# Kernel optimization log

Hardware: AMD Instinct MI355X
Metric: run time of the kernel (lower is better)

## Reference

```python
import jax, jax.numpy as jnp
import numpy as np


def _cdist(x, y):
    # Euclidean (p=2) pairwise distances, matching torch.cdist.
    # x: [B, N, D], y: [B, M, D] -> [B, N, M]
    xx = jnp.sum(x * x, axis=-1)                      # [B, N]
    yy = jnp.sum(y * y, axis=-1)                      # [B, M]
    zz = jnp.einsum('bnd,bmd->bnm', x, y)             # [B, N, M]
    d2 = xx[:, :, None] + yy[:, None, :] - 2.0 * zz
    return jnp.sqrt(jnp.maximum(d2, 0.0))


def setup_inputs() -> dict:
    key = jax.random.key(0)
    k1, k2 = jax.random.split(key)
    gts = jax.random.normal(k1, (4, 8192, 3), dtype=jnp.float32)
    preds = jax.random.normal(k2, (4, 8192, 3), dtype=jnp.float32)
    return {"gts": gts, "preds": preds}


def reference(gts, preds):
    P = _cdist(gts, preds)                 # [B, N, M]
    loss_1 = jnp.sum(jnp.min(P, axis=1), axis=1)  # min over gts points, sum over preds
    loss_2 = jnp.sum(jnp.min(P, axis=2), axis=1)  # min over preds points, sum over gts
    return loss_1 + loss_2                 # [B]
```

## Files before the change

kernel.cpp:

```cpp
#include <hip/hip_runtime.h>
#include <math.h>

#define BB 4
#define NPTS 8192
#define THREADS 256
#define NQ_TOTAL (2 * BB * NPTS)
#define SLICES 4
#define RPS (NPTS / SLICES)
#define QPW 32
#define QPB_MIN (4 * QPW)
#define QGROUPS (NPTS / QPB_MIN)
#define NBLK_MIN (SLICES * 2 * BB * QGROUPS)

typedef __attribute__((ext_vector_type(8)))  short bf16x8;
typedef __attribute__((ext_vector_type(16))) float f32x16;


__device__ __forceinline__ unsigned short f2bf(float f) {
    unsigned u = __float_as_uint(f);
    u += 0x7FFF + ((u >> 16) & 1);
    return (unsigned short)(u >> 16);
}
__device__ __forceinline__ float bf2f(unsigned short h) {
    return __uint_as_float(((unsigned)h) << 16);
}

__global__ __launch_bounds__(THREADS) void pack_kernel(
    const float* __restrict__ gts, const float* __restrict__ preds,
    uint4* __restrict__ refpack, uint4* __restrict__ qpack,
    float* __restrict__ out) {
    int idx = blockIdx.x * THREADS + threadIdx.x;
    if (idx < BB) out[idx] = 0.0f;
    if (idx >= NQ_TOTAL) return;
    int set  = idx / (BB * NPTS);
    int pidx = idx - set * (BB * NPTS);
    const float* src = set ? preds : gts;
    unsigned short hx = f2bf(src[pidx * 3 + 0]);
    unsigned short hy = f2bf(src[pidx * 3 + 1]);
    unsigned short hz = f2bf(src[pidx * 3 + 2]);
    float fx = bf2f(hx), fy = bf2f(hy), fz = bf2f(hz);
    float rr = fmaf(fx, fx, fmaf(fy, fy, fz * fz));
    unsigned short hrr = f2bf(rr);
    unsigned short hlo = f2bf(rr - bf2f(hrr));
    const unsigned short ONE = 0x3F80;

    uint4 rv;
    rv.x = (unsigned)hx  | ((unsigned)hy  << 16);
    rv.y = (unsigned)hz  | ((unsigned)hrr << 16);
    rv.z = (unsigned)hlo | ((unsigned)ONE << 16);
    rv.w = (unsigned)ONE;
    refpack[idx] = rv;

    unsigned short nx = f2bf(-2.0f * fx);
    unsigned short ny = f2bf(-2.0f * fy);
    unsigned short nz = f2bf(-2.0f * fz);
    uint4 qv;
    qv.x = (unsigned)nx  | ((unsigned)ny  << 16);
    qv.y = (unsigned)nz  | ((unsigned)ONE << 16);
    qv.z = (unsigned)ONE | ((unsigned)hrr << 16);
    qv.w = (unsigned)hlo;
    qpack[idx] = qv;
}

__global__ __launch_bounds__(THREADS) void min_kernel(
    const uint4* __restrict__ refpack, const uint4* __restrict__ qpack,
    float* __restrict__ minpart) {
    __shared__ uint4 sref[RPS];

    int tid   = threadIdx.x;
    int blk   = blockIdx.x;
    int slice = blk >> 9;
    int rem   = blk & 511;
    int dir   = rem >> 8;
    int b     = (rem >> 6) & 3;
    int qg    = rem & 63;
    int qset  = dir ^ 1;
    int rset  = dir;

    const uint4* rgl = refpack + (size_t)(rset * BB + b) * NPTS
                     + (size_t)slice * RPS;
    #pragma unroll
    for (int i = 0; i < RPS / THREADS; ++i)
        sref[i * THREADS + tid] = rgl[i * THREADS + tid];
    __syncthreads();

    int wid  = tid >> 6;
    int lane = tid & 63;
    int l31  = lane & 31;
    int half = lane >> 5;

    size_t qoff = (size_t)(qset * BB + b) * NPTS + (size_t)qg * QPB_MIN
                + (size_t)wid * QPW;
    bf16x8 bq = {0, 0, 0, 0, 0, 0, 0, 0};
    if (lane < 32) bq = ((const bf16x8*)qpack)[qoff + l31];

    f32x16 zeroc;
    #pragma unroll
    for (int r = 0; r < 16; ++r) zeroc[r] = 0.0f;

    float macc0 = 3.0e38f, macc1 = 3.0e38f;

    const bf16x8* sp = (const bf16x8*)sref;
    #pragma unroll 4
    for (int t = 0; t < RPS / 64; ++t) {
        bf16x8 a0 = sp[t * 64 + l31];
        bf16x8 a1 = sp[t * 64 + 32 + l31];
        f32x16 d0 = __builtin_amdgcn_mfma_f32_32x32x16_bf16(a0, bq, zeroc, 0, 0, 0);
        f32x16 d1 = __builtin_amdgcn_mfma_f32_32x32x16_bf16(a1, bq, zeroc, 0, 0, 0);
        #pragma unroll
        for (int r = 0; r < 16; r += 2) {
            macc0 = fminf(fminf(d0[r], d0[r + 1]), macc0);
            macc1 = fminf(fminf(d1[r], d1[r + 1]), macc1);
        }
    }

    float macc = fminf(macc0, macc1);
    macc = fminf(macc, __shfl_xor(macc, 32, 64));

    float* mp = minpart + (size_t)slice * NQ_TOTAL
              + (size_t)(dir * BB + b) * NPTS + (size_t)qg * QPB_MIN
              + (size_t)wid * QPW;
    if (lane < 32) mp[l31] = macc;
}

__global__ __launch_bounds__(THREADS) void merge_kernel(
    const float* __restrict__ minpart, float* __restrict__ out) {
    int q = blockIdx.x * THREADS + threadIdx.x;
    float m = minpart[q];
    #pragma unroll
    for (int s = 1; s < SLICES; ++s)
        m = fminf(m, minpart[(size_t)s * NQ_TOTAL + q]);
    float d = sqrtf(fmaxf(m, 0.0f));
    int b = (q >> 13) & 3;

    float sum = d;
    #pragma unroll
    for (int off = 32; off > 0; off >>= 1)
        sum += __shfl_down(sum, off, 64);

    __shared__ float wsum[THREADS / 64];
    int lane = threadIdx.x & 63;
    int wid  = threadIdx.x >> 6;
    if (lane == 0) wsum[wid] = sum;
    __syncthreads();
    if (threadIdx.x == 0)
        atomicAdd(out + b, wsum[0] + wsum[1] + wsum[2] + wsum[3]);
}

extern "C" void kernel_launch(void* const* d_in, const int* in_sizes, int n_in,
                              void* d_out, int out_size, void* d_ws, size_t ws_size,
                              hipStream_t stream) {
    const float* gts   = (const float*)d_in[0];
    const float* preds = (const float*)d_in[1];
    float* out = (float*)d_out;

    char* ws = (char*)d_ws;
    uint4* refpack = (uint4*)ws;
    uint4* qpack   = (uint4*)(ws + (size_t)NQ_TOTAL * 16);
    float* minpart = (float*)(ws + (size_t)NQ_TOTAL * 32);

    pack_kernel<<<NQ_TOTAL / THREADS, THREADS, 0, stream>>>(
        gts, preds, refpack, qpack, out);

    min_kernel<<<NBLK_MIN, THREADS, 0, stream>>>(refpack, qpack, minpart);

    merge_kernel<<<NQ_TOTAL / THREADS, THREADS, 0, stream>>>(minpart, out);
}
```

Baseline: 83.48 us.

## Process 64 queries per wave to reuse each LDS reference load across two MFMAs

Each wave now handles two 32-query B-fragments, so every pair of reference A-fragments read from LDS feeds four MFMAs instead of two. This halves the number of blocks and the total LDS traffic and staging of reference slices per query. In exchange it raises accumulator register pressure (four 16-wide results in flight), lowers the unroll to 2, and halves the grid, which may reduce occupancy and latency hiding.

```diff
diff --git a/kernel.cpp b/kernel.cpp
--- a/kernel.cpp
+++ b/kernel.cpp
@@ -7,7 +7,7 @@
 #define NQ_TOTAL (2 * BB * NPTS)
 #define SLICES 4
 #define RPS (NPTS / SLICES)
-#define QPW 32
+#define QPW 64
 #define QPB_MIN (4 * QPW)
 #define QGROUPS (NPTS / QPB_MIN)
 #define NBLK_MIN (SLICES * 2 * BB * QGROUPS)
@@ -69,11 +69,11 @@
 
     int tid   = threadIdx.x;
     int blk   = blockIdx.x;
-    int slice = blk >> 9;
-    int rem   = blk & 511;
-    int dir   = rem >> 8;
-    int b     = (rem >> 6) & 3;
-    int qg    = rem & 63;
+    int slice = blk >> 8;
+    int rem   = blk & 255;
+    int dir   = rem >> 7;
+    int b     = (rem >> 5) & 3;
+    int qg    = rem & 31;
     int qset  = dir ^ 1;
     int rset  = dir;
 
@@ -87,40 +87,52 @@
     int wid  = tid >> 6;
     int lane = tid & 63;
     int l31  = lane & 31;
-    int half = lane >> 5;
 
     size_t qoff = (size_t)(qset * BB + b) * NPTS + (size_t)qg * QPB_MIN
                 + (size_t)wid * QPW;
-    bf16x8 bq = {0, 0, 0, 0, 0, 0, 0, 0};
-    if (lane < 32) bq = ((const bf16x8*)qpack)[qoff + l31];
+    bf16x8 bq0 = {0, 0, 0, 0, 0, 0, 0, 0};
+    bf16x8 bq1 = {0, 0, 0, 0, 0, 0, 0, 0};
+    if (lane < 32) {
+        bq0 = ((const bf16x8*)qpack)[qoff + l31];
+        bq1 = ((const bf16x8*)qpack)[qoff + 32 + l31];
+    }
 
     f32x16 zeroc;
     #pragma unroll
     for (int r = 0; r < 16; ++r) zeroc[r] = 0.0f;
 
-    float macc0 = 3.0e38f, macc1 = 3.0e38f;
+    float m00 = 3.0e38f, m01 = 3.0e38f, m10 = 3.0e38f, m11 = 3.0e38f;
 
     const bf16x8* sp = (const bf16x8*)sref;
-    #pragma unroll 4
+    #pragma unroll 2
     for (int t = 0; t < RPS / 64; ++t) {
         bf16x8 a0 = sp[t * 64 + l31];
         bf16x8 a1 = sp[t * 64 + 32 + l31];
-        f32x16 d0 = __builtin_amdgcn_mfma_f32_32x32x16_bf16(a0, bq, zeroc, 0, 0, 0);
-        f32x16 d1 = __builtin_amdgcn_mfma_f32_32x32x16_bf16(a1, bq, zeroc, 0, 0, 0);
+        f32x16 d00 = __builtin_amdgcn_mfma_f32_32x32x16_bf16(a0, bq0, zeroc, 0, 0, 0);
+        f32x16 d01 = __builtin_amdgcn_mfma_f32_32x32x16_bf16(a0, bq1, zeroc, 0, 0, 0);
+        f32x16 d10 = __builtin_amdgcn_mfma_f32_32x32x16_bf16(a1, bq0, zeroc, 0, 0, 0);
+        f32x16 d11 = __builtin_amdgcn_mfma_f32_32x32x16_bf16(a1, bq1, zeroc, 0, 0, 0);
         #pragma unroll
         for (int r = 0; r < 16; r += 2) {
-            macc0 = fminf(fminf(d0[r], d0[r + 1]), macc0);
-            macc1 = fminf(fminf(d1[r], d1[r + 1]), macc1);
+            m00 = fminf(fminf(d00[r], d00[r + 1]), m00);
+            m01 = fminf(fminf(d01[r], d01[r + 1]), m01);
+            m10 = fminf(fminf(d10[r], d10[r + 1]), m10);
+            m11 = fminf(fminf(d11[r], d11[r + 1]), m11);
         }
     }
 
-    float macc = fminf(macc0, macc1);
-    macc = fminf(macc, __shfl_xor(macc, 32, 64));
+    float q0 = fminf(m00, m10);
+    float q1 = fminf(m01, m11);
+    q0 = fminf(q0, __shfl_xor(q0, 32, 64));
+    q1 = fminf(q1, __shfl_xor(q1, 32, 64));
 
     float* mp = minpart + (size_t)slice * NQ_TOTAL
               + (size_t)(dir * BB + b) * NPTS + (size_t)qg * QPB_MIN
               + (size_t)wid * QPW;
-    if (lane < 32) mp[l31] = macc;
+    if (lane < 32) {
+        mp[l31]      = q0;
+        mp[l31 + 32] = q1;
+    }
 }
 
 __global__ __launch_bounds__(THREADS) void merge_kernel(
```

After: 83.64 us. Within noise of the previous version (+0.2%).
